# Kernel optimization log

Measured on AMD Instinct MI355X. Metric: run time of the kernel, lower is better.

## Reference

```python
import jax, jax.numpy as jnp
import numpy as np
import math

B, N, T_DIM, K, G = 4, 96, 512, 12, 8


def _normalize(x, eps=1e-6):
    n = jnp.linalg.norm(x, axis=-1, keepdims=True)
    return x / jnp.maximum(n, eps)


def setup_inputs():
    key = jax.random.key(0)
    ks = jax.random.split(key, 12)
    chest_raw = jnp.array([[-0.707, 0.0, 0.707], [0.0, 0.0, 1.0], [0.438, 0.0, 0.899],
                           [0.707, 0.0, 0.707], [0.899, 0.0, 0.438], [0.966, 0.0, 0.259]],
                          dtype=jnp.float32)
    return {
        "mu": jax.random.uniform(ks[0], (B, N), dtype=jnp.float32),
        "sigma0": jax.random.normal(ks[1], (B, N), dtype=jnp.float32) * 0.5,
        "sigma_vel": jax.random.normal(ks[2], (B, N), dtype=jnp.float32) * 0.1,
        "amplitude": jax.random.normal(ks[3], (B, N), dtype=jnp.float32),
        "sh_base": jax.random.normal(ks[4], (B, N, 9), dtype=jnp.float32) * 0.5,
        "sh_vel": jax.random.normal(ks[5], (B, N, 9), dtype=jnp.float32) * 0.1,
        "p0": jax.random.normal(ks[6], (B, N, 3), dtype=jnp.float32) * 0.5,
        "p_vel": jax.random.normal(ks[7], (B, N, 3), dtype=jnp.float32) * 0.2,
        "splat_tau_raw": jnp.asarray(0.0, dtype=jnp.float32),
        "dist_atten_raw": jnp.asarray(-0.5, dtype=jnp.float32),
        "limb_ra": jnp.zeros(3, dtype=jnp.float32),
        "limb_la": jnp.array([1.0, 0.0, 0.0], dtype=jnp.float32),
        "limb_ll": jnp.array([0.5, math.sqrt(3.0) / 2.0, 0.0], dtype=jnp.float32),
        "chest_vectors": chest_raw / jnp.linalg.norm(chest_raw, axis=-1, keepdims=True),
        "conv1_w": jax.random.normal(ks[8], (32, 2, 3, 3), dtype=jnp.float32) * 0.2,
        "conv1_b": jnp.zeros(32, dtype=jnp.float32),
        "conv2_w": jax.random.normal(ks[9], (32, 32, 3, 3), dtype=jnp.float32) * 0.06,
        "conv2_b": jnp.zeros(32, dtype=jnp.float32),
        "fc_w": jax.random.normal(ks[10], (1, 32), dtype=jnp.float32) * 0.2,
        "fc_b": jnp.zeros(1, dtype=jnp.float32),
        "T": T_DIM,
    }


def _conv3x3(x, w, b):
    y = jax.lax.conv_general_dilated(x, w, (1, 1), 'SAME',
                                     dimension_numbers=('NCHW', 'OIHW', 'NCHW'))
    return y + b[None, :, None, None]


def reference(mu, sigma0, sigma_vel, amplitude, sh_base, sh_vel, p0, p_vel,
              splat_tau_raw, dist_atten_raw, limb_ra, limb_la, limb_ll, chest_vectors,
              conv1_w, conv1_b, conv2_w, conv2_b, fc_w, fc_b, T):
    Bq, Nq = mu.shape
    # temporal Gaussian profile
    t = jnp.linspace(0.0, 1.0, T)                                   # (T,)
    dt = t[None, None, :] - mu[:, :, None]                          # (B,N,T)
    sigma_t = jax.nn.softplus(sigma0[:, :, None] + sigma_vel[:, :, None] * dt) + 1e-3
    gauss = amplitude[:, :, None] * jnp.exp(-0.5 * (dt / sigma_t) ** 2)   # (B,N,T)
    sh_dyn = sh_base[:, :, None, :] + sh_vel[:, :, None, :] * dt[..., None]  # (B,N,T,9)

    # dipole position inside the open unit ball
    p_raw = p0[:, :, None, :] + p_vel[:, :, None, :] * dt[..., None]      # (B,N,T,3)
    nrm = jnp.maximum(jnp.linalg.norm(p_raw, axis=-1, keepdims=True), 1e-8)
    p_pos = p_raw / nrm * jnp.tanh(nrm)                                   # (B,N,T,3)

    # limb lead axes from Einthoven triangle (derived every forward)
    L_I = _normalize(limb_la - limb_ra)
    L_II = _normalize(limb_ll - limb_ra)
    L_III = _normalize(limb_ll - limb_la)
    L_aVR = _normalize(limb_ra - (limb_la + limb_ll) * 0.5)
    L_aVL = _normalize(limb_la - (limb_ra + limb_ll) * 0.5)
    L_aVF = _normalize(limb_ll - (limb_ra + limb_la) * 0.5)
    limb = jnp.stack([L_I, L_II, L_III, L_aVR, L_aVL, L_aVF], 0)          # (6,3)
    chest = _normalize(chest_vectors)                                     # (6,3)
    lead = jnp.concatenate([limb, chest], 0)                              # (12,3)
    Lt = jnp.broadcast_to(lead[None, :, None, :], (Bq, 12, T, 3))         # (B,K,T,3)

    # camera-plane orthonormal basis per lead
    a1 = jnp.array([1.0, 0.0, 0.0], dtype=Lt.dtype)
    a2 = jnp.array([0.0, 1.0, 0.0], dtype=Lt.dtype)
    e1 = jnp.cross(Lt, jnp.broadcast_to(a1, Lt.shape))
    small = jnp.linalg.norm(e1, axis=-1, keepdims=True) < 1e-4
    e1 = jnp.where(small, jnp.cross(Lt, jnp.broadcast_to(a2, Lt.shape)), e1)
    e1 = _normalize(e1)
    e2 = _normalize(jnp.cross(e1, Lt))

    # project dipoles onto each lead's image plane
    u = jnp.tanh(jnp.einsum('bntc,bktc->bnkt', p_pos, e1))               # (B,N,K,T)
    v = jnp.tanh(jnp.einsum('bntc,bktc->bnkt', p_pos, e2))

    # spherical-harmonic basis evaluated at lead directions
    x_lv, y_lv, z_lv = Lt[..., 0], Lt[..., 1], Lt[..., 2]                # (B,K,T)
    Y = jnp.stack([0.282095 * jnp.ones_like(x_lv), -0.488603 * y_lv, 0.488603 * z_lv,
                   -0.488603 * x_lv, 1.092548 * x_lv * y_lv, -1.092548 * y_lv * z_lv,
                   0.315392 * (3.0 * z_lv ** 2 - 1.0), -1.092548 * x_lv * z_lv,
                   0.546274 * (x_lv ** 2 - y_lv ** 2)], axis=-1)          # (B,K,T,9)
    sh_proj = jnp.einsum('bntm,bktm->bnkt', sh_dyn, Y)                    # (B,N,K,T)

    tau = jax.nn.softplus(splat_tau_raw) + 0.06
    gamma = jax.nn.softplus(dist_atten_raw) + 1e-6
    p_nrm = jnp.maximum(jnp.linalg.norm(p_pos, axis=-1), 1e-8)            # (B,N,T)
    cosl = jnp.einsum('bntc,bktc->bnkt', p_pos, Lt) / p_nrm[:, :, None, :]
    hem = jnp.maximum(cosl, 0.0)  # halfspace gate (lead_halfspace_gate=True)
    theta = jnp.arccos(jnp.clip(cosl, -1.0 + 1e-6, 1.0 - 1e-6))
    weight = hem * jnp.exp(-gamma * theta * theta)                        # (B,N,K,T)

    # separable splat kernel: exp(-0.5((u-gx)^2+(v-gy)^2)/tau^2) = ku * kv
    grid = jnp.linspace(-1.0, 1.0, G)
    inv2tau2 = 0.5 / (tau * tau)
    ku = jnp.exp(-inv2tau2 * (u[..., None] - grid) ** 2)                  # (B,N,K,T,W)
    kv = jnp.exp(-inv2tau2 * (v[..., None] - grid) ** 2)                  # (B,N,K,T,H)

    A = gauss[:, :, None, :] * weight                                     # (B,N,K,T)
    splat_pos = jnp.einsum('bnkt,bnkth,bnktw->bkthw', A, kv, ku)          # (B,K,T,H,W)
    splat_sh = jnp.einsum('bnkt,bnkth,bnktw->bkthw', A * sh_proj, kv, ku)

    # shared CNN readout over all leads (weights shared)
    x = jnp.stack([splat_pos, splat_sh], axis=3)                          # (B,K,T,2,H,W)
    x = x.reshape(Bq * 12 * T, 2, G, G)
    h = jax.nn.gelu(_conv3x3(x, conv1_w, conv1_b), approximate=False)
    h = jax.nn.gelu(_conv3x3(h, conv2_w, conv2_b), approximate=False)
    h = h.mean(axis=(2, 3))                                               # (B*K*T, 32)
    s = h @ fc_w.T + fc_b                                                 # (B*K*T, 1)
    scalars = s.reshape(Bq, 12, T)                                        # per (b,k,t)
    # faithful to torch: cat(outs,dim=1) -> (B*T,12) then .view(B,12,T)
    V = jnp.transpose(scalars, (0, 2, 1)).reshape(Bq, 12, T)
    return V
```

## Files before the change

kernel.cpp:

```cpp
#include <hip/hip_runtime.h>

#define B_ 4
#define N_ 96
#define T_ 512
#define G_ 8
#define NIMG (B_*12*T_)

typedef _Float16 half8 __attribute__((ext_vector_type(8)));
typedef _Float16 half2t __attribute__((ext_vector_type(2)));
typedef float floatx4 __attribute__((ext_vector_type(4)));
typedef float floatx2 __attribute__((ext_vector_type(2)));

__device__ __forceinline__ float softplusf(float x) {
    return (x > 15.0f) ? x : __logf(1.0f + __expf(x));
}
__device__ __forceinline__ float softplus_small(float x) {
    return __logf(1.0f + __expf(x));
}
__device__ __forceinline__ float fast_tanhf(float x) {
    float ax = fabsf(x);
    float e  = __expf(-2.0f * ax);
    float r  = (1.0f - e) * __builtin_amdgcn_rcpf(1.0f + e);
    return copysignf(r, x);
}
__device__ __forceinline__ float tanh_pade(float x) {
    float x2 = x * x;
    float num = fmaf(x2, x2 + 105.0f, 945.0f);
    float den = fmaf(x2, fmaf(x2, 15.0f, 420.0f), 945.0f);
    return x * num * __builtin_amdgcn_rcpf(den);
}
__device__ __forceinline__ float geluf(float x) {
    float z  = 0.70710678118654752f * x;
    float az = fabsf(z);
    float t  = __builtin_amdgcn_rcpf(fmaf(0.47047f, az, 1.0f));
    float poly = t * fmaf(t, fmaf(t, 0.7478556f, -0.0958798f), 0.3480242f);
    float e  = __expf(-az * az);
    float er = fmaf(-poly, e, 1.0f);
    er = copysignf(er, z);
    return 0.5f * x * (1.0f + er);
}
__device__ __forceinline__ float rfl(float x) {
    return __int_as_float(__builtin_amdgcn_readfirstlane(__float_as_int(x)));
}

__global__ __launch_bounds__(256, 3) void splat_kernel(
    const float* __restrict__ mu,  const float* __restrict__ sg0,
    const float* __restrict__ sgv, const float* __restrict__ amp,
    const float* __restrict__ shb, const float* __restrict__ shv,
    const float* __restrict__ p0,  const float* __restrict__ pv,
    const float* __restrict__ tau_raw, const float* __restrict__ da_raw,
    const float* __restrict__ ra, const float* __restrict__ la,
    const float* __restrict__ ll, const float* __restrict__ chest,
    const float* __restrict__ w1, const float* __restrict__ w2,
    _Float16* __restrict__ outp, _Float16* __restrict__ W1p,
    _Float16* __restrict__ W2p) {
    int lx   = threadIdx.x;
    int nc   = threadIdx.y;
    int flat = nc*64 + lx;
    int tt = lx & 31, ch = lx >> 5;
    int Lb = blockIdx.x;
    int t0 = (Lb & 15) << 5;
    int k  = (Lb >> 4) % 12;
    int b  = Lb / 192;

    if (Lb < 10) {
        for (int e = Lb*1152 + flat; e < Lb*1152 + 1152; e += 256) {
            int tap = e/1280, rem = e - tap*1280, co = rem/40, ci = rem - co*40;
            float val = (ci < 32) ? w2[(co*32+ci)*9 + tap] : 0.0f;
            W2p[e] = (_Float16)val;
        }
    } else if (Lb == 10) {
        for (int e = flat; e < 32*40; e += 256) {
            int co = e/40, kk = e - co*40;
            float val = 0.0f;
            if (kk < 18) { int ci = kk & 1, tap = kk >> 1; val = w1[(co*2+ci)*9 + tap]; }
            W1p[e] = (_Float16)val;
        }
    }

    float vx, vy, vz;
    if      (k == 0) { vx = la[0]-ra[0]; vy = la[1]-ra[1]; vz = la[2]-ra[2]; }
    else if (k == 1) { vx = ll[0]-ra[0]; vy = ll[1]-ra[1]; vz = ll[2]-ra[2]; }
    else if (k == 2) { vx = ll[0]-la[0]; vy = ll[1]-la[1]; vz = ll[2]-la[2]; }
    else if (k == 3) { vx = ra[0]-0.5f*(la[0]+ll[0]); vy = ra[1]-0.5f*(la[1]+ll[1]); vz = ra[2]-0.5f*(la[2]+ll[2]); }
    else if (k == 4) { vx = la[0]-0.5f*(ra[0]+ll[0]); vy = la[1]-0.5f*(ra[1]+ll[1]); vz = la[2]-0.5f*(ra[2]+ll[2]); }
    else if (k == 5) { vx = ll[0]-0.5f*(ra[0]+la[0]); vy = ll[1]-0.5f*(ra[1]+la[1]); vz = ll[2]-0.5f*(ra[2]+la[2]); }
    else             { vx = chest[(k-6)*3+0]; vy = chest[(k-6)*3+1]; vz = chest[(k-6)*3+2]; }
    float nn = fmaxf(sqrtf(vx*vx+vy*vy+vz*vz), 1e-6f);
    float Lx = vx/nn, Ly = vy/nn, Lz = vz/nn;
    float e1x = 0.0f, e1y = Lz, e1z = -Ly;
    if (sqrtf(e1y*e1y + e1z*e1z) < 1e-4f) { e1x = -Lz; e1y = 0.0f; e1z = Lx; }
    float en = fmaxf(sqrtf(e1x*e1x+e1y*e1y+e1z*e1z), 1e-6f);
    e1x /= en; e1y /= en; e1z /= en;
    float e2x = e1y*Lz - e1z*Ly, e2y = e1z*Lx - e1x*Lz, e2z = e1x*Ly - e1y*Lx;
    float fn = fmaxf(sqrtf(e2x*e2x+e2y*e2y+e2z*e2z), 1e-6f);
    e2x /= fn; e2y /= fn; e2z /= fn;
    Lx = rfl(Lx); Ly = rfl(Ly); Lz = rfl(Lz);
    e1x = rfl(e1x); e1y = rfl(e1y); e1z = rfl(e1z);
    e2x = rfl(e2x); e2y = rfl(e2y); e2z = rfl(e2z);
    float Y[9];
    Y[0] = rfl( 0.282095f);
    Y[1] = rfl(-0.488603f*Ly);
    Y[2] = rfl( 0.488603f*Lz);
    Y[3] = rfl(-0.488603f*Lx);
    Y[4] = rfl( 1.092548f*Lx*Ly);
    Y[5] = rfl(-1.092548f*Ly*Lz);
    Y[6] = rfl( 0.315392f*fmaf(3.0f*Lz, Lz, -1.0f));
    Y[7] = rfl(-1.092548f*Lx*Lz);
    Y[8] = rfl( 0.546274f*(Lx*Lx - Ly*Ly));

    float tau = softplusf(tau_raw[0]) + 0.06f;
    float cc2 = rfl(0.5f/(tau*tau));
    float gamma = rfl(softplusf(da_raw[0]) + 1e-6f);
    const float S = 2.0f/7.0f;
    float twoccS = rfl(2.0f*cc2*S);
    float q[8];
#pragma unroll
    for (int w = 0; w < 8; ++w) { float gw = S*(float)w; q[w] = rfl(__expf(-cc2*gw*gw)); }

    float tf = (float)(t0 + tt) * (1.0f/511.0f);
    floatx2 acc2[32];
#pragma unroll
    for (int i = 0; i < 32; ++i) acc2[i] = (floatx2){0.f, 0.f};

    int n0 = nc*24;
    for (int n = n0; n < n0+24; ++n) {
        int base = b*N_ + n;
        float dt  = tf - mu[base];
        float sig = softplus_small(fmaf(sgv[base], dt, sg0[base])) + 1e-3f;
        float z   = dt * __builtin_amdgcn_rcpf(sig);
        float gauss = amp[base] * __expf(-0.5f*z*z);
        float prx = fmaf(pv[base*3+0], dt, p0[base*3+0]);
        float pry = fmaf(pv[base*3+1], dt, p0[base*3+1]);
        float prz = fmaf(pv[base*3+2], dt, p0[base*3+2]);
        float nr  = sqrtf(prx*prx + pry*pry + prz*prz);
        float ncl = fmaxf(nr, 1e-8f);
        float th  = fast_tanhf(ncl);
        float scl = th * __builtin_amdgcn_rcpf(ncl);
        float px = prx*scl, py = pry*scl, pz = prz*scl;
        float pn = fmaxf(th, 1e-8f);
        float cosl = (px*Lx + py*Ly + pz*Lz) * __builtin_amdgcn_rcpf(pn);
        float hem  = fmaxf(cosl, 0.0f);
        if (gauss != 0.0f && hem > 0.0f) {
            float c = fminf(cosl, 0.999999f);
            float s = sqrtf(1.0f - c);
            float theta = s * fmaf(c, fmaf(c, fmaf(c, -0.0187293f, 0.0742610f),
                                   -0.2121144f), 1.5707288f);
            float A = gauss * hem * __expf(-gamma*theta*theta);
            float uu = tanh_pade(px*e1x + py*e1y + pz*e1z);
            float vv = tanh_pade(px*e2x + py*e2y + pz*e2z);
            float Ach = A;
            if (ch) {
                float shp = 0.0f;
#pragma unroll
                for (int m = 0; m < 9; ++m)
                    shp += fmaf(shv[base*9+m], dt, shb[base*9+m]) * Y[m];
                Ach = A * shp;
            }
            float du = uu + 1.0f, dv = vv + 1.0f;
            float bu = __expf(-cc2*du*du);
            float bv = __expf(-cc2*dv*dv);
            float ru = __expf(twoccS*du);
            float rv = __expf(twoccS*dv);
            floatx2 ku2[4];
            float rw = bu;
#pragma unroll
            for (int w = 0; w < 8; ++w) { ku2[w>>1][w&1] = rw*q[w]; rw *= ru; }
            rw = bv;
#pragma unroll
            for (int h = 0; h < 8; ++h) {
                float tp = (rw*q[h])*Ach; rw *= rv;
                floatx2 tp2 = (floatx2){tp, tp};
#pragma unroll
                for (int w2 = 0; w2 < 4; ++w2)
                    acc2[h*4+w2] = __builtin_elementwise_fma(tp2, ku2[w2], acc2[h*4+w2]);
            }
        }
    }

    __shared__ float red[32*132];
    int rbase = tt*132 + ch*64;
    if (nc == 0) {
#pragma unroll
        for (int j = 0; j < 16; ++j) {
            floatx4 v = { acc2[2*j][0], acc2[2*j][1], acc2[2*j+1][0], acc2[2*j+1][1] };
            *(floatx4*)&red[rbase + 4*j] = v;
        }
    }
    __syncthreads();
    if (nc == 1) {
#pragma unroll
        for (int j = 0; j < 16; ++j) {
            floatx4 cur = *(const floatx4*)&red[rbase + 4*j];
            cur[0] += acc2[2*j][0]; cur[1] += acc2[2*j][1];
            cur[2] += acc2[2*j+1][0]; cur[3] += acc2[2*j+1][1];
            *(floatx4*)&red[rbase + 4*j] = cur;
        }
    }
    __syncthreads();
    if (nc == 2) {
#pragma unroll
        for (int j = 0; j < 16; ++j) {
            floatx4 cur = *(const floatx4*)&red[rbase + 4*j];
            cur[0] += acc2[2*j][0]; cur[1] += acc2[2*j][1];
            cur[2] += acc2[2*j+1][0]; cur[3] += acc2[2*j+1][1];
            *(floatx4*)&red[rbase + 4*j] = cur;
        }
    }
    __syncthreads();
    if (nc == 3) {
#pragma unroll
        for (int j = 0; j < 16; ++j) {
            floatx4 cur = *(const floatx4*)&red[rbase + 4*j];
            cur[0] += acc2[2*j][0]; cur[1] += acc2[2*j][1];
            cur[2] += acc2[2*j+1][0]; cur[3] += acc2[2*j+1][1];
            *(floatx4*)&red[rbase + 4*j] = cur;
        }
    }
    __syncthreads();

    int imgbase = (b*12 + k)*T_ + t0;
    int e0 = flat*16, r = e0 >> 7, c0 = e0 & 127;
    half8 h0, h1;
#pragma unroll
    for (int j = 0; j < 8; ++j) {
        h0[j] = (_Float16)red[r*132 + c0 + j];
        h1[j] = (_Float16)red[r*132 + c0 + 8 + j];
    }
    *(half8*)&outp[(imgbase + r)*128 + c0]     = h0;
    *(half8*)&outp[(imgbase + r)*128 + c0 + 8] = h1;
}

__global__ __launch_bounds__(256, 4) void cnn_kernel(
    const _Float16* __restrict__ splat, const _Float16* __restrict__ W1p,
    const _Float16* __restrict__ W2p,  const float* __restrict__ b1,
    const float* __restrict__ b2,      const float* __restrict__ fcw,
    const float* __restrict__ fcb,     float* __restrict__ outv) {
    __shared__ __align__(16) _Float16 sH1[4][100*40];
    __shared__ __align__(16) _Float16 sIn[4][200];
    int tid = threadIdx.x;
    int wv = tid >> 6, lane = tid & 63;
    int img = blockIdx.x*4 + wv;
    _Float16* H  = sH1[wv];
    _Float16* IN = sIn[wv];
    {
        unsigned long long* hz = (unsigned long long*)H;
        for (int i = lane; i < 1000; i += 64) hz[i] = 0ull;
        unsigned int* iz = (unsigned int*)IN;
        for (int i = lane; i < 100; i += 64) iz[i] = 0u;
    }
#pragma unroll
    for (int ii = 0; ii < 2; ++ii) {
        int i = ii*64 + lane;
        int ci = i >> 6, p = i & 63;
        IN[(((p>>3)+1)*10 + (p&7) + 1)*2 + ci] = splat[img*128 + i];
    }
    __syncthreads();

    int r = lane & 15, qd = lane >> 4;
    floatx4 c1[2][4];
#pragma unroll
    for (int nt = 0; nt < 2; ++nt)
#pragma unroll
      for (int mt = 0; mt < 4; ++mt) c1[nt][mt] = (floatx4){0.f,0.f,0.f,0.f};
    half8 bw[2];
#pragma unroll
    for (int nt = 0; nt < 2; ++nt)
        bw[nt] = *(const half8*)&W1p[(nt*16+r)*40 + qd*8];
#pragma unroll
    for (int mt = 0; mt < 4; ++mt) {
        int p = mt*16 + r, py = p>>3, px = p&7;
        half8 a;
#pragma unroll
        for (int m = 0; m < 4; ++m) {
            int tap = qd*4 + m;
            int tc  = (tap > 8) ? 8 : tap;
            int ky = tc/3, kx = tc - ky*3;
            half2t pr = *(const half2t*)&IN[((py+ky)*10 + (px+kx))*2];
            if (tap >= 9) { pr[0] = (_Float16)0.0f; pr[1] = (_Float16)0.0f; }
            a[2*m]   = pr[0];
            a[2*m+1] = pr[1];
        }
#pragma unroll
        for (int nt = 0; nt < 2; ++nt)
            c1[nt][mt] = __builtin_amdgcn_mfma_f32_16x16x32_f16(a, bw[nt], c1[nt][mt], 0, 0, 0);
    }
    float bias1[2] = { b1[r], b1[16+r] };
#pragma unroll
    for (int nt = 0; nt < 2; ++nt)
#pragma unroll
      for (int mt = 0; mt < 4; ++mt)
#pragma unroll
        for (int j = 0; j < 4; ++j) {
            int p = mt*16 + qd*4 + j, py = p>>3, px = p&7;
            float g = geluf(c1[nt][mt][j] + bias1[nt]);
            H[((py+1)*10 + (px+1))*40 + nt*16 + r] = (_Float16)g;
        }
    __syncthreads();
    floatx4 c2[2][4];
#pragma unroll
    for (int nt = 0; nt < 2; ++nt)
#pragma unroll
      for (int mt = 0; mt < 4; ++mt) c2[nt][mt] = (floatx4){0.f,0.f,0.f,0.f};
#pragma unroll
    for (int tap = 0; tap < 9; ++tap) {
        int ky = tap/3, kx = tap - (tap/3)*3;
        half8 wb[2];
#pragma unroll
        for (int nt = 0; nt < 2; ++nt)
            wb[nt] = *(const half8*)&W2p[tap*1280 + (nt*16+r)*40 + qd*8];
#pragma unroll
        for (int mt = 0; mt < 4; ++mt) {
            int p = mt*16 + r, py = p>>3, px = p&7;
            half8 a = *(const half8*)&H[((py+ky)*10 + (px+kx))*40 + qd*8];
#pragma unroll
            for (int nt = 0; nt < 2; ++nt)
                c2[nt][mt] = __builtin_amdgcn_mfma_f32_16x16x32_f16(a, wb[nt], c2[nt][mt], 0, 0, 0);
        }
    }
    float bias2[2] = { b2[r], b2[16+r] };
    float chs0 = 0.f, chs1 = 0.f;
#pragma unroll
    for (int mt = 0; mt < 4; ++mt)
#pragma unroll
      for (int j = 0; j < 4; ++j) {
        chs0 += geluf(c2[0][mt][j] + bias2[0]);
        chs1 += geluf(c2[1][mt][j] + bias2[1]);
      }
    chs0 += __shfl_xor(chs0, 16); chs0 += __shfl_xor(chs0, 32);
    chs1 += __shfl_xor(chs1, 16); chs1 += __shfl_xor(chs1, 32);
    float tot = (chs0 * fcw[r] + chs1 * fcw[16+r]) * (1.0f/64.0f);
    tot += __shfl_xor(tot, 1); tot += __shfl_xor(tot, 2);
    tot += __shfl_xor(tot, 4); tot += __shfl_xor(tot, 8);
    tot += fcb[0];
    if (lane == 0) {
        int t = img & 511, bk = img >> 9;
        int kk = bk % 12, bb = bk / 12;
        outv[(bb*T_ + t)*12 + kk] = tot;
    }
}

extern "C" void kernel_launch(void* const* d_in, const int* in_sizes, int n_in,
                              void* d_out, int out_size, void* d_ws, size_t ws_size,
                              hipStream_t stream) {
    const float* mu   = (const float*)d_in[0];
    const float* sg0  = (const float*)d_in[1];
    const float* sgv  = (const float*)d_in[2];
    const float* amp  = (const float*)d_in[3];
    const float* shb  = (const float*)d_in[4];
    const float* shv  = (const float*)d_in[5];
    const float* p0   = (const float*)d_in[6];
    const float* pvel = (const float*)d_in[7];
    const float* taur = (const float*)d_in[8];
    const float* dar  = (const float*)d_in[9];
    const float* ra   = (const float*)d_in[10];
    const float* la   = (const float*)d_in[11];
    const float* ll   = (const float*)d_in[12];
    const float* chest= (const float*)d_in[13];
    const float* w1   = (const float*)d_in[14];
    const float* b1   = (const float*)d_in[15];
    const float* w2   = (const float*)d_in[16];
    const float* b2   = (const float*)d_in[17];
    const float* fcw  = (const float*)d_in[18];
    const float* fcb  = (const float*)d_in[19];

    char* ws = (char*)d_ws;
    _Float16*  W1p   = (_Float16*)ws;
    _Float16*  W2p   = (_Float16*)(ws + 4096);
    _Float16*  splat = (_Float16*)(ws + 32768);

    splat_kernel<<<768, dim3(64,4), 0, stream>>>(mu, sg0, sgv, amp, shb, shv, p0, pvel,
                                                 taur, dar, ra, la, ll, chest, w1, w2,
                                                 splat, W1p, W2p);
    cnn_kernel<<<NIMG/4, 256, 0, stream>>>(splat, W1p, W2p, b1, b2, fcw, fcb, (float*)d_out);
}
```

Before: 192.2 us.

## Transpose CNN MFMA outputs, fold biases, drop block barriers, use 3-wave blocks

The two conv MFMAs now take weights as the A operand, so each lane holds four consecutive output channels of one pixel. This lets the conv1 GELU results go to LDS as packed half2 stores, and the FC weights are applied per lane before one full-wave shuffle reduction. Biases are loaded as vectors and used as the accumulator initial values rather than added afterwards. Each wave uses only its own LDS slice, so both __syncthreads are removed and blocks shrink to 3 waves via a 2D thread layout. This relies on in-order LDS access within a single wave being enough for correctness in place of the barriers.

```diff
diff --git a/kernel.cpp b/kernel.cpp
--- a/kernel.cpp
+++ b/kernel.cpp
@@ -231,16 +231,15 @@
     *(half8*)&outp[(imgbase + r)*128 + c0 + 8] = h1;
 }
 
-__global__ __launch_bounds__(256, 4) void cnn_kernel(
+__global__ __launch_bounds__(192, 4) void cnn_kernel(
     const _Float16* __restrict__ splat, const _Float16* __restrict__ W1p,
     const _Float16* __restrict__ W2p,  const float* __restrict__ b1,
     const float* __restrict__ b2,      const float* __restrict__ fcw,
     const float* __restrict__ fcb,     float* __restrict__ outv) {
-    __shared__ __align__(16) _Float16 sH1[4][100*40];
-    __shared__ __align__(16) _Float16 sIn[4][200];
-    int tid = threadIdx.x;
-    int wv = tid >> 6, lane = tid & 63;
-    int img = blockIdx.x*4 + wv;
+    __shared__ __align__(16) _Float16 sH1[3][100*40];
+    __shared__ __align__(16) _Float16 sIn[3][200];
+    int wv = threadIdx.y, lane = threadIdx.x;
+    int img = blockIdx.x*3 + wv;
     _Float16* H  = sH1[wv];
     _Float16* IN = sIn[wv];
     {
@@ -255,14 +254,22 @@
         int ci = i >> 6, p = i & 63;
         IN[(((p>>3)+1)*10 + (p&7) + 1)*2 + ci] = splat[img*128 + i];
     }
-    __syncthreads();
 
     int r = lane & 15, qd = lane >> 4;
+    floatx4 b14[2], b24[2], fw4[2];
+#pragma unroll
+    for (int nt = 0; nt < 2; ++nt) {
+        int cb = nt*16 + qd*4;
+        b14[nt] = *(const floatx4*)&b1[cb];
+        b24[nt] = *(const floatx4*)&b2[cb];
+        fw4[nt] = *(const floatx4*)&fcw[cb];
+    }
+
     floatx4 c1[2][4];
 #pragma unroll
     for (int nt = 0; nt < 2; ++nt)
 #pragma unroll
-      for (int mt = 0; mt < 4; ++mt) c1[nt][mt] = (floatx4){0.f,0.f,0.f,0.f};
+      for (int mt = 0; mt < 4; ++mt) c1[nt][mt] = b14[nt];
     half8 bw[2];
 #pragma unroll
     for (int nt = 0; nt < 2; ++nt)
@@ -283,25 +290,28 @@
         }
 #pragma unroll
         for (int nt = 0; nt < 2; ++nt)
-            c1[nt][mt] = __builtin_amdgcn_mfma_f32_16x16x32_f16(a, bw[nt], c1[nt][mt], 0, 0, 0);
-    }
-    float bias1[2] = { b1[r], b1[16+r] };
-#pragma unroll
-    for (int nt = 0; nt < 2; ++nt)
-#pragma unroll
-      for (int mt = 0; mt < 4; ++mt)
-#pragma unroll
-        for (int j = 0; j < 4; ++j) {
-            int p = mt*16 + qd*4 + j, py = p>>3, px = p&7;
-            float g = geluf(c1[nt][mt][j] + bias1[nt]);
-            H[((py+1)*10 + (px+1))*40 + nt*16 + r] = (_Float16)g;
-        }
-    __syncthreads();
+            c1[nt][mt] = __builtin_amdgcn_mfma_f32_16x16x32_f16(bw[nt], a, c1[nt][mt], 0, 0, 0);
+    }
+#pragma unroll
+    for (int nt = 0; nt < 2; ++nt)
+#pragma unroll
+      for (int mt = 0; mt < 4; ++mt) {
+        int p = mt*16 + r, py = p>>3, px = p&7;
+        int hb = ((py+1)*10 + (px+1))*40 + nt*16 + qd*4;
+        half2t h01, h23;
+        h01[0] = (_Float16)geluf(c1[nt][mt][0]);
+        h01[1] = (_Float16)geluf(c1[nt][mt][1]);
+        h23[0] = (_Float16)geluf(c1[nt][mt][2]);
+        h23[1] = (_Float16)geluf(c1[nt][mt][3]);
+        *(half2t*)&H[hb]     = h01;
+        *(half2t*)&H[hb + 2] = h23;
+      }
+
     floatx4 c2[2][4];
 #pragma unroll
     for (int nt = 0; nt < 2; ++nt)
 #pragma unroll
-      for (int mt = 0; mt < 4; ++mt) c2[nt][mt] = (floatx4){0.f,0.f,0.f,0.f};
+      for (int mt = 0; mt < 4; ++mt) c2[nt][mt] = b24[nt];
 #pragma unroll
     for (int tap = 0; tap < 9; ++tap) {
         int ky = tap/3, kx = tap - (tap/3)*3;
@@ -315,23 +325,21 @@
             half8 a = *(const half8*)&H[((py+ky)*10 + (px+kx))*40 + qd*8];
 #pragma unroll
             for (int nt = 0; nt < 2; ++nt)
-                c2[nt][mt] = __builtin_amdgcn_mfma_f32_16x16x32_f16(a, wb[nt], c2[nt][mt], 0, 0, 0);
-        }
-    }
-    float bias2[2] = { b2[r], b2[16+r] };
-    float chs0 = 0.f, chs1 = 0.f;
-#pragma unroll
-    for (int mt = 0; mt < 4; ++mt)
-#pragma unroll
-      for (int j = 0; j < 4; ++j) {
-        chs0 += geluf(c2[0][mt][j] + bias2[0]);
-        chs1 += geluf(c2[1][mt][j] + bias2[1]);
-      }
-    chs0 += __shfl_xor(chs0, 16); chs0 += __shfl_xor(chs0, 32);
-    chs1 += __shfl_xor(chs1, 16); chs1 += __shfl_xor(chs1, 32);
-    float tot = (chs0 * fcw[r] + chs1 * fcw[16+r]) * (1.0f/64.0f);
-    tot += __shfl_xor(tot, 1); tot += __shfl_xor(tot, 2);
-    tot += __shfl_xor(tot, 4); tot += __shfl_xor(tot, 8);
+                c2[nt][mt] = __builtin_amdgcn_mfma_f32_16x16x32_f16(wb[nt], a, c2[nt][mt], 0, 0, 0);
+        }
+    }
+    float tot = 0.f;
+#pragma unroll
+    for (int nt = 0; nt < 2; ++nt)
+#pragma unroll
+      for (int mt = 0; mt < 4; ++mt)
+#pragma unroll
+        for (int j = 0; j < 4; ++j)
+            tot = fmaf(geluf(c2[nt][mt][j]), fw4[nt][j], tot);
+    tot *= (1.0f/64.0f);
+    tot += __shfl_xor(tot, 1);  tot += __shfl_xor(tot, 2);
+    tot += __shfl_xor(tot, 4);  tot += __shfl_xor(tot, 8);
+    tot += __shfl_xor(tot, 16); tot += __shfl_xor(tot, 32);
     tot += fcb[0];
     if (lane == 0) {
         int t = img & 511, bk = img >> 9;
@@ -372,5 +380,6 @@
     splat_kernel<<<768, dim3(64,4), 0, stream>>>(mu, sg0, sgv, amp, shb, shv, p0, pvel,
                                                  taur, dar, ra, la, ll, chest, w1, w2,
                                                  splat, W1p, W2p);
-    cnn_kernel<<<NIMG/4, 256, 0, stream>>>(splat, W1p, W2p, b1, b2, fcw, fcb, (float*)d_out);
-}
+    cnn_kernel<<<NIMG/3, dim3(64,3), 0, stream>>>(splat, W1p, W2p, b1, b2, fcw, fcb,
+                                                  (float*)d_out);
+}
```

New measurement: 194.4 us. About the same (+1.1%).
